# Optimization experiments

Hardware: AMD Instinct MI355X
Metric: run time of the kernel (lower is better)

Reference implementation:

```python
import jax, jax.numpy as jnp
import numpy as np
from jax import lax

D_MODEL = 384
D_STATE = 16
D_CONV = 4
EXPAND = 2
D_INNER = EXPAND * D_MODEL            # 768
DT_RANK = int(np.ceil(D_INNER / 16))  # 48
B_SZ, L_SEQ = 8, 1024
LN_EPS = 1e-5


def setup_inputs() -> dict:
    key = jax.random.key(0)
    ks = jax.random.split(key, 10)
    x = jax.random.normal(ks[0], (B_SZ, L_SEQ, D_MODEL), dtype=jnp.float32)
    ln_g = jnp.ones((D_MODEL,), jnp.float32)
    ln_b = jnp.zeros((D_MODEL,), jnp.float32)
    in_proj_w = jax.random.normal(ks[1], (2 * D_INNER, D_MODEL), jnp.float32) * (D_MODEL ** -0.5)
    conv_w = jax.random.normal(ks[2], (D_INNER, 1, D_CONV), jnp.float32) * (D_CONV ** -0.5)
    conv_b = jax.random.normal(ks[3], (D_INNER,), jnp.float32) * 0.01
    x_proj_w = jax.random.normal(ks[4], (DT_RANK + 2 * D_STATE, D_INNER), jnp.float32) * (D_INNER ** -0.5)
    dt_std = DT_RANK ** -0.5
    dt_proj_w = jax.random.uniform(ks[5], (D_INNER, DT_RANK), jnp.float32, -dt_std, dt_std)
    dt_proj_b = jax.random.normal(ks[6], (D_INNER,), jnp.float32) * 0.01
    A_log = jnp.log(jnp.tile(jnp.arange(1, D_STATE + 1, dtype=jnp.float32), (D_INNER, 1)))
    D_param = jnp.ones((D_INNER,), jnp.float32)
    out_proj_w = jax.random.normal(ks[7], (D_MODEL, D_INNER), jnp.float32) * (D_INNER ** -0.5)
    return {"x": x, "ln_g": ln_g, "ln_b": ln_b, "in_proj_w": in_proj_w,
            "conv_w": conv_w, "conv_b": conv_b, "x_proj_w": x_proj_w,
            "dt_proj_w": dt_proj_w, "dt_proj_b": dt_proj_b, "A_log": A_log,
            "D_param": D_param, "out_proj_w": out_proj_w}


def _selective_scan(u, delta, A, Bm, Cm):
    # u, delta: (B,L,Din); A: (Din,N); Bm, Cm: (B,L,N)
    dA = jnp.exp(delta[..., None] * A)                 # (B,L,Din,N)
    dBu = (delta * u)[..., None] * Bm[:, :, None, :]   # (B,L,Din,N)
    dA_t = jnp.moveaxis(dA, 1, 0)                      # (L,B,Din,N)
    dBu_t = jnp.moveaxis(dBu, 1, 0)
    C_t = jnp.moveaxis(Cm, 1, 0)                       # (L,B,N)

    def step(h, inp):
        dA_s, dBu_s, c_s = inp
        h = dA_s * h + dBu_s                           # (B,Din,N)
        y = jnp.einsum('bdn,bn->bd', h, c_s)
        return h, y

    h0 = jnp.zeros((u.shape[0], u.shape[2], A.shape[1]), u.dtype)
    _, ys = lax.scan(step, h0, (dA_t, dBu_t, C_t))
    return jnp.moveaxis(ys, 0, 1)                      # (B,L,Din)


def reference(x, ln_g, ln_b, in_proj_w, conv_w, conv_b, x_proj_w,
              dt_proj_w, dt_proj_b, A_log, D_param, out_proj_w):
    residual = x
    # LayerNorm
    mu = jnp.mean(x, axis=-1, keepdims=True)
    var = jnp.var(x, axis=-1, keepdims=True)
    xn = (x - mu) * lax.rsqrt(var + LN_EPS) * ln_g + ln_b
    # in_proj and split
    xz = xn @ in_proj_w.T                              # (B,L,2*Din)
    xh, z = jnp.split(xz, 2, axis=-1)
    # causal depthwise conv1d (torch pads both sides then truncates to L)
    xc = lax.conv_general_dilated(
        jnp.moveaxis(xh, 1, 2), conv_w, (1,), [(D_CONV - 1, 0)],
        feature_group_count=D_INNER,
        dimension_numbers=('NCH', 'OIH', 'NCH')) + conv_b[None, :, None]
    u = jax.nn.silu(jnp.moveaxis(xc, 1, 2))            # (B,L,Din)
    # SSM input-dependent params
    xpo = u @ x_proj_w.T                               # (B,L,dt_rank+2N)
    dlow, Bm, Cm = jnp.split(xpo, [DT_RANK, DT_RANK + D_STATE], axis=-1)
    delta = jax.nn.softplus(dlow @ dt_proj_w.T + dt_proj_b)
    A = -jnp.exp(A_log)
    y = _selective_scan(u, delta, A, Bm, Cm)
    y = y + u * D_param
    y = y * jax.nn.silu(z)
    out = y @ out_proj_w.T
    return residual + out
```

## Files before the change

### kernel.cpp

```cpp
#include <hip/hip_runtime.h>
#include <math.h>

#define DMODEL 384
#define DIN 768
#define NST 16
#define DTR 48
#define BSZ 8
#define LSEQ 1024
#define NROWS (BSZ*LSEQ)
#define XPO_W (DTR + 2*NST)
#define CL 64
#define NC (LSEQ/CL)
#define CSEG 32

typedef __attribute__((ext_vector_type(8))) short bf16x8;
typedef __attribute__((ext_vector_type(4))) float f32x4;

__device__ __forceinline__ unsigned short f2bf(float x) {
  unsigned int u = __float_as_uint(x);
  unsigned int r = u + 0x7fffu + ((u >> 16) & 1u);
  return (unsigned short)(r >> 16);
}
__device__ __forceinline__ float bf2f(unsigned short h) {
  return __uint_as_float(((unsigned int)h) << 16);
}

__device__ __forceinline__ void gll16(const void* g, void* l) {
  __builtin_amdgcn_global_load_lds(
      (const __attribute__((address_space(1))) void*)g,
      (__attribute__((address_space(3))) void*)l, 16, 0, 0);
}

__global__ __launch_bounds__(256) void ln_kernel(const float* __restrict__ x,
    const float* __restrict__ g, const float* __restrict__ b,
    unsigned short* __restrict__ xh, unsigned short* __restrict__ xl) {
  int row = blockIdx.x * 4 + (threadIdx.x >> 6);
  int lane = threadIdx.x & 63;
  const float* xr = x + (size_t)row * DMODEL;
  float v[6];
  float s = 0.f, ss = 0.f;
#pragma unroll
  for (int i = 0; i < 6; ++i) { v[i] = xr[lane + i*64]; s += v[i]; ss += v[i]*v[i]; }
#pragma unroll
  for (int off = 32; off; off >>= 1) { s += __shfl_xor(s, off); ss += __shfl_xor(ss, off); }
  float mu = s * (1.f / DMODEL);
  float var = ss * (1.f / DMODEL) - mu * mu;
  float inv = rsqrtf(var + 1e-5f);
#pragma unroll
  for (int i = 0; i < 6; ++i) {
    int c = lane + i*64;
    float o = (v[i] - mu) * inv * g[c] + b[c];
    unsigned short hv = f2bf(o);
    xh[(size_t)row*DMODEL + c] = hv;
    xl[(size_t)row*DMODEL + c] = f2bf(o - bf2f(hv));
  }
}

__device__ __forceinline__ void split_one(const float* src, int ldsrc, int R, int C,
    unsigned short* dh, unsigned short* dl, int Cpad, int i) {
  int r = i / Cpad, c = i - r * Cpad;
  float v = (r < R && c < C) ? src[(size_t)r*ldsrc + c] : 0.f;
  unsigned short hv = f2bf(v);
  dh[i] = hv;
  dl[i] = f2bf(v - bf2f(hv));
}
#define N_INW (1536*384)
#define N_XW  (128*768)
#define N_DTW (768*64)
#define N_OW  (384*768)
__global__ __launch_bounds__(256) void split_weights(
    const float* __restrict__ inw, const float* __restrict__ xw,
    const float* __restrict__ dtw, const float* __restrict__ ow,
    unsigned short* inw_h, unsigned short* inw_l,
    unsigned short* xw_h, unsigned short* xw_l,
    unsigned short* dtw_h, unsigned short* dtw_l,
    unsigned short* ow_h, unsigned short* ow_l) {
  int i = blockIdx.x * 256 + threadIdx.x;
  if (i < N_INW) { split_one(inw, 384, 1536, 384, inw_h, inw_l, 384, i); return; }
  i -= N_INW;
  if (i < N_XW)  { split_one(xw, 768, 80, 768, xw_h, xw_l, 768, i); return; }
  i -= N_XW;
  if (i < N_DTW) { split_one(dtw, 48, 768, 48, dtw_h, dtw_l, 64, i); return; }
  i -= N_DTW;
  if (i < N_OW)  { split_one(ow, 768, 384, 768, ow_h, ow_l, 768, i); return; }
}

template<int EPI>
__global__ __launch_bounds__(256, 2) void gemm_mfma(
    const unsigned short* __restrict__ Ah, const unsigned short* __restrict__ Al, int lda,
    const unsigned short* __restrict__ Bh, const unsigned short* __restrict__ Bl, int ldb,
    float* __restrict__ C, int ldc, size_t strideS,
    const float* __restrict__ bias, const float* __restrict__ res,
    int T) {
  __shared__ unsigned short lds[2][4][4096];
  int tid = threadIdx.x;
  int lane = tid & 63, wid = tid >> 6;
  int wm = wid >> 1, wn = wid & 1;

  unsigned nwg = gridDim.x * gridDim.y;
  unsigned bid = blockIdx.y * gridDim.x + blockIdx.x;
  unsigned cpx = nwg >> 3;
  unsigned sw = (bid & 7) * cpx + (bid >> 3);
  unsigned bx = sw % gridDim.x, by = sw / gridDim.x;
  int m0 = by * 128, n0 = bx * 128;
  C += (size_t)blockIdx.z * strideS;
  size_t kofs = (size_t)blockIdx.z * T * 32;

  f32x4 acc[4][4];
#pragma unroll
  for (int i = 0; i < 4; ++i)
#pragma unroll
    for (int j = 0; j < 4; ++j) acc[i][j] = (f32x4){0.f, 0.f, 0.f, 0.f};

  int kgl = lane >> 4, rl = lane & 15;

  int c0 = wid*128 + lane;
  int c1 = wid*128 + 64 + lane;
  int r0 = c0 & 127, kg0 = c0 >> 7;
  int r1 = c1 & 127, kg1 = c1 >> 7;

#define STAGE(bf, kt) do { \
    size_t ga0 = (size_t)(m0 + r0) * lda + (kt) + kg0*8 + kofs; \
    size_t gb0 = (size_t)(n0 + r0) * ldb + (kt) + kg0*8 + kofs; \
    size_t ga1 = (size_t)(m0 + r1) * lda + (kt) + kg1*8 + kofs; \
    size_t gb1 = (size_t)(n0 + r1) * ldb + (kt) + kg1*8 + kofs; \
    gll16(Ah + ga0, &lds[bf][0][(wid*128)*8]); \
    gll16(Al + ga0, &lds[bf][1][(wid*128)*8]); \
    gll16(Bh + gb0, &lds[bf][2][(wid*128)*8]); \
    gll16(Bl + gb0, &lds[bf][3][(wid*128)*8]); \
    gll16(Ah + ga1, &lds[bf][0][(wid*128+64)*8]); \
    gll16(Al + ga1, &lds[bf][1][(wid*128+64)*8]); \
    gll16(Bh + gb1, &lds[bf][2][(wid*128+64)*8]); \
    gll16(Bl + gb1, &lds[bf][3][(wid*128+64)*8]); \
  } while (0)

  STAGE(0, 0);
  asm volatile("s_waitcnt vmcnt(0)" ::: "memory");
  __builtin_amdgcn_s_barrier();

  int cur = 0;
  for (int t = 0; t < T; ++t) {
    if (t + 1 < T) {
      STAGE(cur ^ 1, (t + 1) << 5);
    }
    asm volatile("" ::: "memory");
    bf16x8 ah[4], al[4], bh[4], bl[4];
#pragma unroll
    for (int mi = 0; mi < 4; ++mi) {
      int cell = kgl*128 + wm*64 + mi*16 + rl;
      ah[mi] = *reinterpret_cast<const bf16x8*>(&lds[cur][0][cell*8]);
      al[mi] = *reinterpret_cast<const bf16x8*>(&lds[cur][1][cell*8]);
    }
#pragma unroll
    for (int ni = 0; ni < 4; ++ni) {
      int cell = kgl*128 + wn*64 + ni*16 + rl;
      bh[ni] = *reinterpret_cast<const bf16x8*>(&lds[cur][2][cell*8]);
      bl[ni] = *reinterpret_cast<const bf16x8*>(&lds[cur][3][cell*8]);
    }
#pragma unroll
    for (int mi = 0; mi < 4; ++mi)
#pragma unroll
      for (int ni = 0; ni < 4; ++ni) {
        acc[mi][ni] = __builtin_amdgcn_mfma_f32_16x16x32_bf16(ah[mi], bh[ni], acc[mi][ni], 0, 0, 0);
        acc[mi][ni] = __builtin_amdgcn_mfma_f32_16x16x32_bf16(al[mi], bh[ni], acc[mi][ni], 0, 0, 0);
        acc[mi][ni] = __builtin_amdgcn_mfma_f32_16x16x32_bf16(ah[mi], bl[ni], acc[mi][ni], 0, 0, 0);
      }
    asm volatile("s_waitcnt vmcnt(0)" ::: "memory");
    __builtin_amdgcn_s_barrier();
    cur ^= 1;
  }
#undef STAGE

#pragma unroll
  for (int mi = 0; mi < 4; ++mi)
#pragma unroll
    for (int ni = 0; ni < 4; ++ni)
#pragma unroll
      for (int j = 0; j < 4; ++j) {
        int m = m0 + wm*64 + mi*16 + (lane>>4)*4 + j;
        int n = n0 + wn*64 + ni*16 + (lane&15);
        float v = acc[mi][ni][j];
        if (EPI == 0) {
          C[(size_t)m*ldc + n] = v;
        } else if (EPI == 2) {
          v += bias[n];
          v = (v > 20.f) ? v : log1pf(__expf(v));
          C[(size_t)m*ldc + n] = v;
        } else if (EPI == 3) {
          C[(size_t)m*ldc + n] = v + res[(size_t)m*ldc + n];
        }
      }
}

__global__ __launch_bounds__(256) void reduce_xproj(
    const float* __restrict__ P, float* __restrict__ xpo,
    unsigned short* __restrict__ dh, unsigned short* __restrict__ dl) {
  int idx = blockIdx.x * 256 + threadIdx.x;
  int m = idx >> 7, n = idx & 127;
  float v = 0.f;
#pragma unroll
  for (int s = 0; s < 4; ++s) v += P[(size_t)s * NROWS * 128 + idx];
  if (n < XPO_W) xpo[(size_t)m * XPO_W + n] = v;
  if (n < 64) {
    unsigned short hv = f2bf(v);
    dh[(size_t)m*64 + n] = hv;
    dl[(size_t)m*64 + n] = f2bf(v - bf2f(hv));
  }
}

__global__ __launch_bounds__(256) void reduce_out(
    const float* __restrict__ P, const float* __restrict__ x, float* __restrict__ out) {
  int i = blockIdx.x * 256 + threadIdx.x;
  out[i] = x[i] + P[i] + P[i + (size_t)NROWS*DMODEL];
}

__global__ __launch_bounds__(256) void conv_silu_kernel(
    const float* __restrict__ xz, const float* __restrict__ w,
    const float* __restrict__ cb,
    unsigned short* __restrict__ uh, unsigned short* __restrict__ ul) {
  int d = blockIdx.x * 256 + threadIdx.x;
  int l0 = blockIdx.y * CSEG;
  int b = blockIdx.z;
  float xv[CSEG + 3];
#pragma unroll
  for (int i = 0; i < CSEG + 3; ++i) {
    int l = l0 + i - 3;
    xv[i] = (l >= 0) ? xz[((size_t)b*LSEQ + l) * (2*DIN) + d] : 0.f;
  }
  float w0 = w[d*4], w1 = w[d*4+1], w2 = w[d*4+2], w3 = w[d*4+3];
  float cbv = cb[d];
#pragma unroll
  for (int i = 0; i < CSEG; ++i) {
    float acc = cbv;
    acc = fmaf(xv[i],     w0, acc);
    acc = fmaf(xv[i + 1], w1, acc);
    acc = fmaf(xv[i + 2], w2, acc);
    acc = fmaf(xv[i + 3], w3, acc);
    float s = acc / (1.f + __expf(-acc));
    size_t idx = ((size_t)b*LSEQ + l0 + i) * DIN + d;
    unsigned short hv = f2bf(s);
    uh[idx] = hv;
    ul[idx] = f2bf(s - bf2f(hv));
  }
}

__global__ __launch_bounds__(256) void scan_pass1(
    const float* __restrict__ delta,
    const unsigned short* __restrict__ uh, const unsigned short* __restrict__ ul,
    const float* __restrict__ xpo, const float* __restrict__ A_log,
    float* __restrict__ carryA, float* __restrict__ carryH) {
  int d = blockIdx.x * 256 + threadIdx.x;
  int c = blockIdx.y, b = blockIdx.z;
  float A[16];
  {
    const float4* al = reinterpret_cast<const float4*>(A_log + (size_t)d * NST);
#pragma unroll
    for (int i = 0; i < 4; ++i) {
      float4 t = al[i];
      A[4*i+0] = -__expf(t.x); A[4*i+1] = -__expf(t.y);
      A[4*i+2] = -__expf(t.z); A[4*i+3] = -__expf(t.w);
    }
  }
  float h[16], ap[16];
#pragma unroll
  for (int n = 0; n < 16; ++n) { h[n] = 0.f; ap[n] = 1.f; }
  const float* dp = delta + ((size_t)b*LSEQ + c*CL) * DIN + d;
  const unsigned short* uhp = uh + ((size_t)b*LSEQ + c*CL) * DIN + d;
  const unsigned short* ulp = ul + ((size_t)b*LSEQ + c*CL) * DIN + d;
  const float* bp = xpo   + ((size_t)b*LSEQ + c*CL) * XPO_W + DTR;
  for (int l = 0; l < CL; ++l) {
    float dv = dp[(size_t)l*DIN];
    float uv = bf2f(uhp[(size_t)l*DIN]) + bf2f(ulp[(size_t)l*DIN]);
    float du = dv * uv;
    float Bv[16];
    {
      const float4* b4 = reinterpret_cast<const float4*>(bp + (size_t)l*XPO_W);
#pragma unroll
      for (int i = 0; i < 4; ++i) {
        float4 t = b4[i];
        Bv[4*i+0] = t.x; Bv[4*i+1] = t.y; Bv[4*i+2] = t.z; Bv[4*i+3] = t.w;
      }
    }
#pragma unroll
    for (int n = 0; n < 16; ++n) {
      float a = __expf(dv * A[n]);
      ap[n] *= a;
      h[n] = fmaf(a, h[n], du * Bv[n]);
    }
  }
  size_t ci = (((size_t)b*NC + c) * DIN + d) * NST;
  float4* ca = reinterpret_cast<float4*>(carryA + ci);
  float4* ch = reinterpret_cast<float4*>(carryH + ci);
#pragma unroll
  for (int i = 0; i < 4; ++i) {
    ca[i] = make_float4(ap[4*i], ap[4*i+1], ap[4*i+2], ap[4*i+3]);
    ch[i] = make_float4(h[4*i],  h[4*i+1],  h[4*i+2],  h[4*i+3]);
  }
}

__global__ __launch_bounds__(256) void scan_mid(
    const float* __restrict__ carryA, float* __restrict__ carryH) {
  int idx = blockIdx.x * 256 + threadIdx.x;
  int b = idx / (DIN*NST);
  int rem = idx - b * DIN*NST;
  float h = 0.f;
#pragma unroll
  for (int c = 0; c < NC; ++c) {
    size_t i = ((size_t)b*NC + c) * (DIN*NST) + rem;
    float a = carryA[i];
    float e = carryH[i];
    carryH[i] = h;
    h = fmaf(a, h, e);
  }
}

__global__ __launch_bounds__(256) void scan_pass2(
    const float* __restrict__ delta,
    const unsigned short* __restrict__ uh, const unsigned short* __restrict__ ul,
    const float* __restrict__ xpo, const float* __restrict__ xz,
    const float* __restrict__ A_log, const float* __restrict__ Dp,
    const float* __restrict__ carryH,
    unsigned short* __restrict__ yh, unsigned short* __restrict__ yl) {
  int d = blockIdx.x * 256 + threadIdx.x;
  int c = blockIdx.y, b = blockIdx.z;
  float A[16];
  {
    const float4* al = reinterpret_cast<const float4*>(A_log + (size_t)d * NST);
#pragma unroll
    for (int i = 0; i < 4; ++i) {
      float4 t = al[i];
      A[4*i+0] = -__expf(t.x); A[4*i+1] = -__expf(t.y);
      A[4*i+2] = -__expf(t.z); A[4*i+3] = -__expf(t.w);
    }
  }
  float h[16];
  size_t ci = (((size_t)b*NC + c) * DIN + d) * NST;
  {
    const float4* ch = reinterpret_cast<const float4*>(carryH + ci);
#pragma unroll
    for (int i = 0; i < 4; ++i) {
      float4 t = ch[i];
      h[4*i+0] = t.x; h[4*i+1] = t.y; h[4*i+2] = t.z; h[4*i+3] = t.w;
    }
  }
  float Dd = Dp[d];
  const float* dp = delta + ((size_t)b*LSEQ + c*CL) * DIN + d;
  const unsigned short* uhp = uh + ((size_t)b*LSEQ + c*CL) * DIN + d;
  const unsigned short* ulp = ul + ((size_t)b*LSEQ + c*CL) * DIN + d;
  const float* bp = xpo   + ((size_t)b*LSEQ + c*CL) * XPO_W + DTR;
  const float* zp = xz    + ((size_t)b*LSEQ + c*CL) * (2*DIN) + DIN + d;
  size_t yi0 = ((size_t)b*LSEQ + c*CL) * DIN + d;
  for (int l = 0; l < CL; ++l) {
    float dv = dp[(size_t)l*DIN];
    float uv = bf2f(uhp[(size_t)l*DIN]) + bf2f(ulp[(size_t)l*DIN]);
    float du = dv * uv;
    float Bv[16], Cv[16];
    {
      const float4* b4 = reinterpret_cast<const float4*>(bp + (size_t)l*XPO_W);
#pragma unroll
      for (int i = 0; i < 4; ++i) {
        float4 t = b4[i];
        Bv[4*i+0] = t.x; Bv[4*i+1] = t.y; Bv[4*i+2] = t.z; Bv[4*i+3] = t.w;
        float4 tc = b4[i+4];
        Cv[4*i+0] = tc.x; Cv[4*i+1] = tc.y; Cv[4*i+2] = tc.z; Cv[4*i+3] = tc.w;
      }
    }
    float p = 0.f;
#pragma unroll
    for (int n = 0; n < 16; ++n) {
      float a = __expf(dv * A[n]);
      h[n] = fmaf(a, h[n], du * Bv[n]);
      p = fmaf(h[n], Cv[n], p);
    }
    float z = zp[(size_t)l*(2*DIN)];
    float sz = z / (1.f + __expf(-z));
    float yv = fmaf(uv, Dd, p) * sz;
    unsigned short hv = f2bf(yv);
    yh[yi0 + (size_t)l*DIN] = hv;
    yl[yi0 + (size_t)l*DIN] = f2bf(yv - bf2f(hv));
  }
}

extern "C" void kernel_launch(void* const* d_in, const int* in_sizes, int n_in,
                              void* d_out, int out_size, void* d_ws, size_t ws_size,
                              hipStream_t stream) {
  const float* x          = (const float*)d_in[0];
  const float* ln_g       = (const float*)d_in[1];
  const float* ln_b       = (const float*)d_in[2];
  const float* in_proj_w  = (const float*)d_in[3];
  const float* conv_w     = (const float*)d_in[4];
  const float* conv_b     = (const float*)d_in[5];
  const float* x_proj_w   = (const float*)d_in[6];
  const float* dt_proj_w  = (const float*)d_in[7];
  const float* dt_proj_b  = (const float*)d_in[8];
  const float* A_log      = (const float*)d_in[9];
  const float* D_param    = (const float*)d_in[10];
  const float* out_proj_w = (const float*)d_in[11];

  char* w = (char*)d_ws;
  unsigned short* xn_h  = (unsigned short*)w;
  unsigned short* xn_l  = xn_h + (size_t)NROWS*DMODEL;
  unsigned short* dlow_h = (unsigned short*)w;
  unsigned short* dlow_l = dlow_h + (size_t)NROWS*64;
  float* carryA = (float*)w;
  float* carryH = carryA + (size_t)BSZ*NC*DIN*NST;
  char* p = w + (size_t)NROWS*DMODEL*4;
  float* xz = (float*)p;              p += (size_t)NROWS*2*DIN*4;
  unsigned short* u_h = (unsigned short*)p;
  unsigned short* u_l = u_h + (size_t)NROWS*DIN;      p += (size_t)NROWS*DIN*4;
  float* xpo = (float*)p;             p += (size_t)NROWS*XPO_W*4;
  float* delta = (float*)p;           p += (size_t)NROWS*DIN*4;
  unsigned short* inw_h = (unsigned short*)delta;
  unsigned short* inw_l = inw_h + (size_t)1536*384;
  unsigned short* xw_h  = inw_l + (size_t)1536*384;
  unsigned short* xw_l  = xw_h + (size_t)128*768;
  unsigned short* y2_h = (unsigned short*)p;
  unsigned short* y2_l = y2_h + (size_t)NROWS*DIN;
  float* xpart = (float*)p;           p += (size_t)NROWS*DIN*4;
  unsigned short* dtw_h = (unsigned short*)p;
  unsigned short* dtw_l = dtw_h + (size_t)768*64;
  unsigned short* ow_h  = dtw_l + (size_t)768*64;
  unsigned short* ow_l  = ow_h + (size_t)384*768;
  float* opart = xz;

  split_weights<<<(N_INW+N_XW+N_DTW+N_OW)/256, 256, 0, stream>>>(
      in_proj_w, x_proj_w, dt_proj_w, out_proj_w,
      inw_h, inw_l, xw_h, xw_l, dtw_h, dtw_l, ow_h, ow_l);

  ln_kernel<<<NROWS/4, 256, 0, stream>>>(x, ln_g, ln_b, xn_h, xn_l);

  gemm_mfma<0><<<dim3(12, 64, 1), 256, 0, stream>>>(xn_h, xn_l, DMODEL, inw_h, inw_l, DMODEL,
      xz, 2*DIN, 0, nullptr, nullptr, 12);

  conv_silu_kernel<<<dim3(DIN/256, LSEQ/CSEG, BSZ), 256, 0, stream>>>(
      xz, conv_w, conv_b, u_h, u_l);

  gemm_mfma<0><<<dim3(1, 64, 4), 256, 0, stream>>>(u_h, u_l, DIN, xw_h, xw_l, DIN,
      xpart, 128, (size_t)NROWS*128, nullptr, nullptr, 6);
  reduce_xproj<<<(NROWS*128)/256, 256, 0, stream>>>(xpart, xpo, dlow_h, dlow_l);

  gemm_mfma<2><<<dim3(6, 64, 1), 256, 0, stream>>>(dlow_h, dlow_l, 64, dtw_h, dtw_l, 64,
      delta, DIN, 0, dt_proj_b, nullptr, 2);

  {
    dim3 g1(DIN/256, NC, BSZ);
    scan_pass1<<<g1, 256, 0, stream>>>(delta, u_h, u_l, xpo, A_log, carryA, carryH);
    scan_mid<<<(BSZ*DIN*NST)/256, 256, 0, stream>>>(carryA, carryH);
    scan_pass2<<<g1, 256, 0, stream>>>(delta, u_h, u_l, xpo, xz, A_log, D_param,
                                       carryH, y2_h, y2_l);
  }

  gemm_mfma<0><<<dim3(3, 64, 2), 256, 0, stream>>>(y2_h, y2_l, DIN, ow_h, ow_l, DIN,
      opart, DMODEL, (size_t)NROWS*DMODEL, nullptr, nullptr, 12);
  reduce_out<<<(NROWS*DMODEL)/256, 256, 0, stream>>>(opart, x, (float*)d_out);
}
```

Baseline: 249.9 us.

## Load GEMM A operands straight to registers, stage only B in LDS

The split-bf16 GEMM now loads the A tile (hi/lo) directly from global memory into double-buffered registers, with each wave loading only its own rows. Only the B tile goes through LDS, which halves LDS traffic and footprint per block. It also fully unrolls the K loop with T as a template parameter, raises wave priority around the MFMA block, and replaces the full vmcnt(0) wait with a partial vmcnt wait. The trade-off is more VGPRs for the register buffers and global A loads that are less coalesced and duplicated across the waves sharing wm.

```diff
diff --git a/kernel.cpp b/kernel.cpp
--- a/kernel.cpp
+++ b/kernel.cpp
@@ -85,14 +85,13 @@
   if (i < N_OW)  { split_one(ow, 768, 384, 768, ow_h, ow_l, 768, i); return; }
 }
 
-template<int EPI>
-__global__ __launch_bounds__(256, 2) void gemm_mfma(
+template<int EPI, int T>
+__global__ __launch_bounds__(256, 2) void gemm_rp(
     const unsigned short* __restrict__ Ah, const unsigned short* __restrict__ Al, int lda,
     const unsigned short* __restrict__ Bh, const unsigned short* __restrict__ Bl, int ldb,
     float* __restrict__ C, int ldc, size_t strideS,
-    const float* __restrict__ bias, const float* __restrict__ res,
-    int T) {
-  __shared__ unsigned short lds[2][4][4096];
+    const float* __restrict__ bias) {
+  __shared__ unsigned short lds[2][2][4096];
   int tid = threadIdx.x;
   int lane = tid & 63, wid = tid >> 6;
   int wm = wid >> 1, wn = wid & 1;
@@ -106,70 +105,84 @@
   C += (size_t)blockIdx.z * strideS;
   size_t kofs = (size_t)blockIdx.z * T * 32;
 
-  f32x4 acc[4][4];
-#pragma unroll
-  for (int i = 0; i < 4; ++i)
-#pragma unroll
-    for (int j = 0; j < 4; ++j) acc[i][j] = (f32x4){0.f, 0.f, 0.f, 0.f};
-
   int kgl = lane >> 4, rl = lane & 15;
+
+  const unsigned short* pAh[4];
+  const unsigned short* pAl[4];
+#pragma unroll
+  for (int mi = 0; mi < 4; ++mi) {
+    size_t off = (size_t)(m0 + wm*64 + mi*16 + rl) * lda + kgl*8 + kofs;
+    pAh[mi] = Ah + off;
+    pAl[mi] = Al + off;
+  }
 
   int c0 = wid*128 + lane;
   int c1 = wid*128 + 64 + lane;
   int r0 = c0 & 127, kg0 = c0 >> 7;
   int r1 = c1 & 127, kg1 = c1 >> 7;
 
-#define STAGE(bf, kt) do { \
-    size_t ga0 = (size_t)(m0 + r0) * lda + (kt) + kg0*8 + kofs; \
+#define STAGEB(bf, kt) do { \
     size_t gb0 = (size_t)(n0 + r0) * ldb + (kt) + kg0*8 + kofs; \
-    size_t ga1 = (size_t)(m0 + r1) * lda + (kt) + kg1*8 + kofs; \
     size_t gb1 = (size_t)(n0 + r1) * ldb + (kt) + kg1*8 + kofs; \
-    gll16(Ah + ga0, &lds[bf][0][(wid*128)*8]); \
-    gll16(Al + ga0, &lds[bf][1][(wid*128)*8]); \
-    gll16(Bh + gb0, &lds[bf][2][(wid*128)*8]); \
-    gll16(Bl + gb0, &lds[bf][3][(wid*128)*8]); \
-    gll16(Ah + ga1, &lds[bf][0][(wid*128+64)*8]); \
-    gll16(Al + ga1, &lds[bf][1][(wid*128+64)*8]); \
-    gll16(Bh + gb1, &lds[bf][2][(wid*128+64)*8]); \
-    gll16(Bl + gb1, &lds[bf][3][(wid*128+64)*8]); \
+    gll16(Bh + gb0, &lds[bf][0][(wid*128)*8]); \
+    gll16(Bl + gb0, &lds[bf][1][(wid*128)*8]); \
+    gll16(Bh + gb1, &lds[bf][0][(wid*128+64)*8]); \
+    gll16(Bl + gb1, &lds[bf][1][(wid*128+64)*8]); \
   } while (0)
 
-  STAGE(0, 0);
-  asm volatile("s_waitcnt vmcnt(0)" ::: "memory");
+#define LOADA(p, kt) do { \
+    _Pragma("unroll") \
+    for (int mi = 0; mi < 4; ++mi) { \
+      arh[p][mi] = *reinterpret_cast<const bf16x8*>(pAh[mi] + (kt)); \
+      arl[p][mi] = *reinterpret_cast<const bf16x8*>(pAl[mi] + (kt)); \
+    } \
+  } while (0)
+
+  f32x4 acc[4][4];
+#pragma unroll
+  for (int i = 0; i < 4; ++i)
+#pragma unroll
+    for (int j = 0; j < 4; ++j) acc[i][j] = (f32x4){0.f, 0.f, 0.f, 0.f};
+
+  bf16x8 arh[2][4], arl[2][4];
+
+  STAGEB(0, 0);
+  LOADA(0, 0);
+  asm volatile("s_waitcnt vmcnt(8)" ::: "memory");
   __builtin_amdgcn_s_barrier();
 
-  int cur = 0;
+#pragma unroll
   for (int t = 0; t < T; ++t) {
+    int cur = t & 1, nxt = (t + 1) & 1;
     if (t + 1 < T) {
-      STAGE(cur ^ 1, (t + 1) << 5);
-    }
-    asm volatile("" ::: "memory");
-    bf16x8 ah[4], al[4], bh[4], bl[4];
-#pragma unroll
-    for (int mi = 0; mi < 4; ++mi) {
-      int cell = kgl*128 + wm*64 + mi*16 + rl;
-      ah[mi] = *reinterpret_cast<const bf16x8*>(&lds[cur][0][cell*8]);
-      al[mi] = *reinterpret_cast<const bf16x8*>(&lds[cur][1][cell*8]);
-    }
+      STAGEB(nxt, (t + 1) * 32);
+      LOADA(nxt, (t + 1) * 32);
+    }
+    bf16x8 bh[4], bl[4];
 #pragma unroll
     for (int ni = 0; ni < 4; ++ni) {
       int cell = kgl*128 + wn*64 + ni*16 + rl;
-      bh[ni] = *reinterpret_cast<const bf16x8*>(&lds[cur][2][cell*8]);
-      bl[ni] = *reinterpret_cast<const bf16x8*>(&lds[cur][3][cell*8]);
-    }
+      bh[ni] = *reinterpret_cast<const bf16x8*>(&lds[cur][0][cell*8]);
+      bl[ni] = *reinterpret_cast<const bf16x8*>(&lds[cur][1][cell*8]);
+    }
+    __builtin_amdgcn_s_setprio(1);
 #pragma unroll
     for (int mi = 0; mi < 4; ++mi)
 #pragma unroll
       for (int ni = 0; ni < 4; ++ni) {
-        acc[mi][ni] = __builtin_amdgcn_mfma_f32_16x16x32_bf16(ah[mi], bh[ni], acc[mi][ni], 0, 0, 0);
-        acc[mi][ni] = __builtin_amdgcn_mfma_f32_16x16x32_bf16(al[mi], bh[ni], acc[mi][ni], 0, 0, 0);
-        acc[mi][ni] = __builtin_amdgcn_mfma_f32_16x16x32_bf16(ah[mi], bl[ni], acc[mi][ni], 0, 0, 0);
+        acc[mi][ni] = __builtin_amdgcn_mfma_f32_16x16x32_bf16(arh[cur][mi], bh[ni], acc[mi][ni], 0, 0, 0);
+        acc[mi][ni] = __builtin_amdgcn_mfma_f32_16x16x32_bf16(arl[cur][mi], bh[ni], acc[mi][ni], 0, 0, 0);
+        acc[mi][ni] = __builtin_amdgcn_mfma_f32_16x16x32_bf16(arh[cur][mi], bl[ni], acc[mi][ni], 0, 0, 0);
       }
-    asm volatile("s_waitcnt vmcnt(0)" ::: "memory");
-    __builtin_amdgcn_s_barrier();
-    cur ^= 1;
-  }
-#undef STAGE
+    __builtin_amdgcn_s_setprio(0);
+    if (t + 1 < T) {
+      asm volatile("s_waitcnt vmcnt(8) lgkmcnt(0)" ::: "memory");
+      __builtin_amdgcn_sched_barrier(0);
+      __builtin_amdgcn_s_barrier();
+    }
+  }
+#undef STAGEB
+#undef LOADA
 
 #pragma unroll
   for (int mi = 0; mi < 4; ++mi)
@@ -178,7 +191,7 @@
 #pragma unroll
       for (int j = 0; j < 4; ++j) {
         int m = m0 + wm*64 + mi*16 + (lane>>4)*4 + j;
-        int n = n0 + wn*64 + ni*16 + (lane&15);
+        int n = n0 + wn*64 + ni*16 + rl;
         float v = acc[mi][ni][j];
         if (EPI == 0) {
           C[(size_t)m*ldc + n] = v;
@@ -186,8 +199,6 @@
           v += bias[n];
           v = (v > 20.f) ? v : log1pf(__expf(v));
           C[(size_t)m*ldc + n] = v;
-        } else if (EPI == 3) {
-          C[(size_t)m*ldc + n] = v + res[(size_t)m*ldc + n];
         }
       }
 }
@@ -429,18 +440,18 @@
 
   ln_kernel<<<NROWS/4, 256, 0, stream>>>(x, ln_g, ln_b, xn_h, xn_l);
 
-  gemm_mfma<0><<<dim3(12, 64, 1), 256, 0, stream>>>(xn_h, xn_l, DMODEL, inw_h, inw_l, DMODEL,
-      xz, 2*DIN, 0, nullptr, nullptr, 12);
+  gemm_rp<0, 12><<<dim3(12, 64, 1), 256, 0, stream>>>(xn_h, xn_l, DMODEL,
+      inw_h, inw_l, DMODEL, xz, 2*DIN, 0, nullptr);
 
   conv_silu_kernel<<<dim3(DIN/256, LSEQ/CSEG, BSZ), 256, 0, stream>>>(
       xz, conv_w, conv_b, u_h, u_l);
 
-  gemm_mfma<0><<<dim3(1, 64, 4), 256, 0, stream>>>(u_h, u_l, DIN, xw_h, xw_l, DIN,
-      xpart, 128, (size_t)NROWS*128, nullptr, nullptr, 6);
+  gemm_rp<0, 6><<<dim3(1, 64, 4), 256, 0, stream>>>(u_h, u_l, DIN,
+      xw_h, xw_l, DIN, xpart, 128, (size_t)NROWS*128, nullptr);
   reduce_xproj<<<(NROWS*128)/256, 256, 0, stream>>>(xpart, xpo, dlow_h, dlow_l);
 
-  gemm_mfma<2><<<dim3(6, 64, 1), 256, 0, stream>>>(dlow_h, dlow_l, 64, dtw_h, dtw_l, 64,
-      delta, DIN, 0, dt_proj_b, nullptr, 2);
+  gemm_rp<2, 2><<<dim3(6, 64, 1), 256, 0, stream>>>(dlow_h, dlow_l, 64,
+      dtw_h, dtw_l, 64, delta, DIN, 0, dt_proj_b);
 
   {
     dim3 g1(DIN/256, NC, BSZ);
@@ -450,7 +461,7 @@
                                        carryH, y2_h, y2_l);
   }
 
-  gemm_mfma<0><<<dim3(3, 64, 2), 256, 0, stream>>>(y2_h, y2_l, DIN, ow_h, ow_l, DIN,
-      opart, DMODEL, (size_t)NROWS*DMODEL, nullptr, nullptr, 12);
+  gemm_rp<0, 12><<<dim3(3, 64, 2), 256, 0, stream>>>(y2_h, y2_l, DIN,
+      ow_h, ow_l, DIN, opart, DMODEL, (size_t)NROWS*DMODEL, nullptr);
   reduce_out<<<(NROWS*DMODEL)/256, 256, 0, stream>>>(opart, x, (float*)d_out);
 }
```

Result: slower. 276.0 us (+10.4%).
